# Optimization experiments

Hardware: AMD Instinct MI355X
Metric: run time of the kernel (lower is better)

The kernel has to match this reference:

```python
import jax, jax.numpy as jnp
import numpy as np
from jax import lax

B, C_IN, H, W = 16, 64, 112, 112
OUP = 128
INIT = 64          # ceil(oup/ratio)
NEW = 64           # init*(ratio-1)
E = 4              # num_experts
SE_HID = (INIT + NEW) // 4
EPS = 1e-5


def setup_inputs() -> dict:
    key = jax.random.key(0)
    ks = jax.random.split(key, 12)
    n = jax.random.normal
    d = {}
    d["x"] = n(ks[0], (B, C_IN, H, W), jnp.float32)
    # DynamicConv 1 (1x1, experts)
    d["rw1"] = n(ks[1], (E, C_IN), jnp.float32) * 0.1
    d["rb1"] = jnp.zeros((E,), jnp.float32)
    d["w1"] = n(ks[2], (E, INIT, C_IN, 1, 1), jnp.float32) / np.sqrt(C_IN)
    d["bn1_g"] = jnp.ones((INIT,), jnp.float32)
    d["bn1_b"] = jnp.zeros((INIT,), jnp.float32)
    d["bn1_m"] = n(ks[3], (INIT,), jnp.float32) * 0.1
    d["bn1_v"] = jax.random.uniform(ks[4], (INIT,), jnp.float32, 0.5, 1.5)
    # DynamicConv 2 (3x3 depthwise, experts)
    d["rw2"] = n(ks[5], (E, INIT), jnp.float32) * 0.1
    d["rb2"] = jnp.zeros((E,), jnp.float32)
    d["w2"] = n(ks[6], (E, NEW, 1, 3, 3), jnp.float32) / 3.0
    d["bn2_g"] = jnp.ones((NEW,), jnp.float32)
    d["bn2_b"] = jnp.zeros((NEW,), jnp.float32)
    d["bn2_m"] = n(ks[7], (NEW,), jnp.float32) * 0.1
    d["bn2_v"] = jax.random.uniform(ks[8], (NEW,), jnp.float32, 0.5, 1.5)
    # AdaptiveSE on INIT+NEW channels
    d["se_w1"] = n(ks[9], (SE_HID, INIT + NEW), jnp.float32) * 0.1
    d["se_b1"] = jnp.zeros((SE_HID,), jnp.float32)
    d["se_w2"] = n(ks[10], (INIT + NEW, SE_HID), jnp.float32) * 0.1
    d["se_b2"] = jnp.zeros((INIT + NEW,), jnp.float32)
    return d


def _bn_relu(x, g, b, m, v):
    # eval-mode BatchNorm2d + ReLU, channel dim = 1
    scale = (g / jnp.sqrt(v + EPS))[None, :, None, None]
    shift = (b - m * g / jnp.sqrt(v + EPS))[None, :, None, None]
    return jax.nn.relu(x * scale + shift)


def reference(x, rw1, rb1, w1, bn1_g, bn1_b, bn1_m, bn1_v,
              rw2, rb2, w2, bn2_g, bn2_b, bn2_m, bn2_v,
              se_w1, se_b1, se_w2, se_b2):
    b = x.shape[0]
    # --- first block: dynamic 1x1 conv ---
    pooled = x.mean((2, 3))                                  # [B, C_IN]
    r1 = jax.nn.sigmoid(pooled @ rw1.T + rb1)                # [B, E]
    # per-sample mixed 1x1 kernel: [B, INIT, C_IN]
    k1 = jnp.einsum('be,eoi->boi', r1, w1[:, :, :, 0, 0])
    x1 = jnp.einsum('boi,bihw->bohw', k1, x)                 # [B, INIT, H, W]
    x1 = _bn_relu(x1, bn1_g, bn1_b, bn1_m, bn1_v)
    # --- second block: dynamic 3x3 depthwise conv ---
    pooled2 = x1.mean((2, 3))                                # [B, INIT]
    r2 = jax.nn.sigmoid(pooled2 @ rw2.T + rb2)               # [B, E]
    k2 = jnp.einsum('be,eokl->bokl', r2, w2[:, :, 0])        # [B, NEW, 3, 3]
    # batched grouped conv: groups = B*INIT (CondConv trick)
    x1r = x1.reshape(1, b * INIT, H, W)
    k2r = k2.reshape(b * NEW, 1, 3, 3)
    x2 = lax.conv_general_dilated(
        x1r, k2r, window_strides=(1, 1), padding=((1, 1), (1, 1)),
        dimension_numbers=('NCHW', 'OIHW', 'NCHW'),
        feature_group_count=b * INIT)
    x2 = x2.reshape(b, NEW, H, W)
    x2 = _bn_relu(x2, bn2_g, bn2_b, bn2_m, bn2_v)
    # --- concat + SE gate ---
    out = jnp.concatenate([x1, x2], axis=1)                  # [B, INIT+NEW, H, W]
    s = out.mean((2, 3))                                     # [B, INIT+NEW]
    s = jax.nn.relu(s @ se_w1.T + se_b1)
    s = jax.nn.sigmoid(s @ se_w2.T + se_b2)
    out = out * s[:, :, None, None]
    return out[:, :OUP]
```

## Files before the change

kernel.cpp:

```cpp
#include <hip/hip_runtime.h>
#include <math.h>

#define NB 16
#define CIN 64
#define HH 112
#define WW 112
#define HW 12544
#define INIT_C 64
#define NEW_C 64
#define NE 4
#define SE_HIDN 32
#define OUTC 128
#define EPSV 1e-5f
#define TPX 256
#define NT (HW / TPX)

__global__ __launch_bounds__(256) void k_pool(const float* __restrict__ x,
                                              float* __restrict__ pooled,
                                              float* __restrict__ sum1) {
    int bc = blockIdx.x;
    const float4* p4 = (const float4*)(x + (size_t)bc * HW);
    float s = 0.f;
    for (int g = threadIdx.x; g < HW / 4; g += 256) {
        float4 v = p4[g];
        s += v.x + v.y + v.z + v.w;
    }
    for (int off = 32; off > 0; off >>= 1) s += __shfl_down(s, off, 64);
    __shared__ float ls[4];
    if ((threadIdx.x & 63) == 0) ls[threadIdx.x >> 6] = s;
    __syncthreads();
    if (threadIdx.x == 0) {
        pooled[bc] = (ls[0] + ls[1] + ls[2] + ls[3]) * (1.f / (float)HW);
        sum1[bc] = 0.f;
    }
}

__global__ __launch_bounds__(256) void k_prep(
    const float* __restrict__ pooled, const float* __restrict__ rw1,
    const float* __restrict__ rb1, const float* __restrict__ w1,
    const float* __restrict__ bn1_g, const float* __restrict__ bn1_v,
    float* __restrict__ k1t) {
    int b = blockIdx.x;
    int t = threadIdx.x;
    __shared__ float r1s[NE];
    if (t < NE) {
        float acc = rb1[t];
        const float* pb = pooled + b * CIN;
        const float* rw = rw1 + t * CIN;
        for (int i = 0; i < CIN; i++) acc = fmaf(pb[i], rw[i], acc);
        r1s[t] = 1.f / (1.f + expf(-acc));
    }
    __syncthreads();
    for (int idx = t; idx < CIN * INIT_C; idx += 256) {
        int o = idx & 63, i = idx >> 6;
        float acc = 0.f;
#pragma unroll
        for (int e = 0; e < NE; e++)
            acc = fmaf(r1s[e], w1[(e * INIT_C + o) * CIN + i], acc);
        float sc = bn1_g[o] * rsqrtf(bn1_v[o] + EPSV);
        k1t[b * (CIN * INIT_C) + idx] = acc * sc;
    }
}

__global__ __launch_bounds__(256, 2) void k_conv1(
    const float* __restrict__ x, const float* __restrict__ k1t,
    const float* __restrict__ bn1_g, const float* __restrict__ bn1_b,
    const float* __restrict__ bn1_m, const float* __restrict__ bn1_v,
    float* __restrict__ out, float* __restrict__ sum1) {
    __shared__ alignas(16) float sA[CIN * INIT_C];
    __shared__ alignas(16) float sX[CIN * TPX];
    __shared__ float sShift[INIT_C];
    int b = blockIdx.x / NT;
    int tile = blockIdx.x % NT;
    int p0 = tile * TPX;
    int t = threadIdx.x;

    {
        const float4* src = (const float4*)(k1t + (size_t)b * CIN * INIT_C);
        for (int g = t; g < CIN * INIT_C / 4; g += 256) ((float4*)sA)[g] = src[g];
    }
    if (t < INIT_C) {
        float sc = bn1_g[t] * rsqrtf(bn1_v[t] + EPSV);
        sShift[t] = bn1_b[t] - bn1_m[t] * sc;
    }
    {
        const float* gx = x + (size_t)b * CIN * HW + p0;
        for (int g = t; g < CIN * TPX / 4; g += 256) {
            int i = g >> 6, c4 = g & 63;
            ((float4*)sX)[g] = *(const float4*)(gx + (size_t)i * HW + (c4 << 2));
        }
    }
    __syncthreads();

    int og = t >> 5;
    int pg = t & 31;
    float acc[8][8];
#pragma unroll
    for (int u = 0; u < 8; u++)
#pragma unroll
        for (int v = 0; v < 8; v++) acc[u][v] = 0.f;

    const float4* sA4 = (const float4*)sA;
    const float4* sX4 = (const float4*)sX;
#pragma unroll 2
    for (int i = 0; i < CIN; i++) {
        float4 a0 = sA4[i * (INIT_C / 4) + og * 2];
        float4 a1 = sA4[i * (INIT_C / 4) + og * 2 + 1];
        float4 x0 = sX4[i * (TPX / 4) + pg];
        float4 x1 = sX4[i * (TPX / 4) + 32 + pg];
        float av[8] = {a0.x, a0.y, a0.z, a0.w, a1.x, a1.y, a1.z, a1.w};
        float xv[8] = {x0.x, x0.y, x0.z, x0.w, x1.x, x1.y, x1.z, x1.w};
#pragma unroll
        for (int u = 0; u < 8; u++)
#pragma unroll
            for (int v = 0; v < 8; v++)
                acc[u][v] = fmaf(av[u], xv[v], acc[u][v]);
    }

    float csum[8];
#pragma unroll
    for (int u = 0; u < 8; u++) {
        int o = og * 8 + u;
        float sh = sShift[o];
        alignas(16) float r0[4], r1[4];
#pragma unroll
        for (int v = 0; v < 4; v++) {
            r0[v] = fmaxf(acc[u][v] + sh, 0.f);
            r1[v] = fmaxf(acc[u][4 + v] + sh, 0.f);
        }
        float* dst = out + ((size_t)(b * OUTC + o)) * HW + p0;
        *(float4*)(dst + pg * 4) = *(float4*)r0;
        *(float4*)(dst + 128 + pg * 4) = *(float4*)r1;
        csum[u] = r0[0] + r0[1] + r0[2] + r0[3] + r1[0] + r1[1] + r1[2] + r1[3];
    }
#pragma unroll
    for (int u = 0; u < 8; u++) {
        float v = csum[u];
        v += __shfl_xor(v, 16, 64);
        v += __shfl_xor(v, 8, 64);
        v += __shfl_xor(v, 4, 64);
        v += __shfl_xor(v, 2, 64);
        v += __shfl_xor(v, 1, 64);
        if (pg == 0) atomicAdd(&sum1[b * INIT_C + og * 8 + u], v);
    }
}

__device__ __forceinline__ void ldrow(const float* __restrict__ sP, int pr,
                                      int cg, float4& C, float& L, float& R) {
    const float* row = sP + pr * WW;
    C = *(const float4*)(row + cg * 4);
    int lc = cg * 4 - 1;
    lc = lc < 0 ? 0 : lc;
    float lv = row[lc];
    L = (cg == 0) ? 0.f : lv;
    int rc = cg * 4 + 4;
    rc = rc > (WW - 1) ? (WW - 1) : rc;
    float rv = row[rc];
    R = (cg == 27) ? 0.f : rv;
}

__device__ __forceinline__ float4 dw9(const float4 c0, float l0, float r0,
                                      const float4 c1, float l1, float r1,
                                      const float4 c2, float l2, float r2,
                                      const float* __restrict__ K) {
    float4 o;
    o.x = fmaf(K[0], l0, fmaf(K[1], c0.x, fmaf(K[2], c0.y,
          fmaf(K[3], l1, fmaf(K[4], c1.x, fmaf(K[5], c1.y,
          fmaf(K[6], l2, fmaf(K[7], c2.x, K[8] * c2.y))))))));
    o.y = fmaf(K[0], c0.x, fmaf(K[1], c0.y, fmaf(K[2], c0.z,
          fmaf(K[3], c1.x, fmaf(K[4], c1.y, fmaf(K[5], c1.z,
          fmaf(K[6], c2.x, fmaf(K[7], c2.y, K[8] * c2.z))))))));
    o.z = fmaf(K[0], c0.y, fmaf(K[1], c0.z, fmaf(K[2], c0.w,
          fmaf(K[3], c1.y, fmaf(K[4], c1.z, fmaf(K[5], c1.w,
          fmaf(K[6], c2.y, fmaf(K[7], c2.z, K[8] * c2.w))))))));
    o.w = fmaf(K[0], c0.z, fmaf(K[1], c0.w, fmaf(K[2], r0,
          fmaf(K[3], c1.z, fmaf(K[4], c1.w, fmaf(K[5], r1,
          fmaf(K[6], c2.z, fmaf(K[7], c2.w, K[8] * r2))))))));
    return o;
}

#define PROWS (HH + 2)

__global__ __launch_bounds__(256) void k_dwsum(
    const float* __restrict__ xin, const float* __restrict__ sum1,
    const float* __restrict__ rw2, const float* __restrict__ rb2,
    const float* __restrict__ w2, const float* __restrict__ bn2_g,
    const float* __restrict__ bn2_b, const float* __restrict__ bn2_m,
    const float* __restrict__ bn2_v, float* __restrict__ sum2) {
    __shared__ alignas(16) float sP[PROWS * WW];
    __shared__ float r2s[NE];
    __shared__ float kks[9];
    int c = blockIdx.x & 63;
    int b = blockIdx.x >> 6;
    int t = threadIdx.x;

    if (t < NE) {
        float acc = rb2[t];
        const float* s1 = sum1 + b * INIT_C;
        const float* rw = rw2 + t * INIT_C;
        for (int i = 0; i < INIT_C; i++)
            acc = fmaf(s1[i] * (1.f / (float)HW), rw[i], acc);
        r2s[t] = 1.f / (1.f + expf(-acc));
    }
    if (t < WW / 4) {
        float4 z = {0.f, 0.f, 0.f, 0.f};
        ((float4*)sP)[t] = z;
        ((float4*)(sP + (PROWS - 1) * WW))[t] = z;
    }
    __syncthreads();
    if (t < 9) {
        float acc = 0.f;
#pragma unroll
        for (int e = 0; e < NE; e++)
            acc = fmaf(r2s[e], w2[(e * NEW_C + c) * 9 + t], acc);
        kks[t] = acc * (bn2_g[c] * rsqrtf(bn2_v[c] + EPSV));
    }
    const float4* src4 = (const float4*)(xin + ((size_t)(b * OUTC + c)) * HW);
    float4* dst4 = (float4*)(sP + WW);
    for (int g = t; g < HW / 4; g += 256) dst4[g] = src4[g];
    __syncthreads();

    float sc2 = bn2_g[c] * rsqrtf(bn2_v[c] + EPSV);
    float shift = bn2_b[c] - bn2_m[c] * sc2;
    float myk[9];
#pragma unroll
    for (int j = 0; j < 9; j++) myk[j] = kks[j];

    int cg = t & 31;
    int band = t >> 5;
    float csum = 0.f;
    if (cg < 28) {
        int pr0 = band * 14;
        float4 C[3];
        float L[3], R[3];
        ldrow(sP, pr0, cg, C[0], L[0], R[0]);
        ldrow(sP, pr0 + 1, cg, C[1], L[1], R[1]);
#pragma unroll
        for (int k = 0; k < 14; k++) {
            int s0 = k % 3, s1 = (k + 1) % 3, s2 = (k + 2) % 3;
            ldrow(sP, pr0 + k + 2, cg, C[s2], L[s2], R[s2]);
            float4 o = dw9(C[s0], L[s0], R[s0], C[s1], L[s1], R[s1],
                           C[s2], L[s2], R[s2], myk);
            csum += fmaxf(o.x + shift, 0.f) + fmaxf(o.y + shift, 0.f) +
                    fmaxf(o.z + shift, 0.f) + fmaxf(o.w + shift, 0.f);
        }
    }
    for (int off = 32; off > 0; off >>= 1) csum += __shfl_down(csum, off, 64);
    __shared__ float ls[4];
    if ((t & 63) == 0) ls[t >> 6] = csum;
    __syncthreads();
    if (t == 0) sum2[b * NEW_C + c] = ls[0] + ls[1] + ls[2] + ls[3];
}

__global__ __launch_bounds__(256) void k_final(
    const float* __restrict__ xin, const float* __restrict__ sum1,
    const float* __restrict__ sum2, const float* __restrict__ rw2,
    const float* __restrict__ rb2, const float* __restrict__ w2,
    const float* __restrict__ bn2_g, const float* __restrict__ bn2_b,
    const float* __restrict__ bn2_m, const float* __restrict__ bn2_v,
    const float* __restrict__ se_w1, const float* __restrict__ se_b1,
    const float* __restrict__ se_w2, const float* __restrict__ se_b2,
    float* __restrict__ out) {
    __shared__ alignas(16) float sP[PROWS * WW];
    __shared__ float sin_[OUTC];
    __shared__ float hvec[SE_HIDN];
    __shared__ float r2s[NE];
    __shared__ float kks[9];
    int c = blockIdx.x & 63;
    int b = blockIdx.x >> 6;
    int t = threadIdx.x;

    if (t < 64) sin_[t] = sum1[b * 64 + t] * (1.f / (float)HW);
    else if (t < 128) sin_[t] = sum2[b * 64 + (t - 64)] * (1.f / (float)HW);
    if (t >= 128 && t < 128 + NE) {
        int e = t - 128;
        float acc = rb2[e];
        const float* s1 = sum1 + b * INIT_C;
        const float* rw = rw2 + e * INIT_C;
        for (int i = 0; i < INIT_C; i++)
            acc = fmaf(s1[i] * (1.f / (float)HW), rw[i], acc);
        r2s[e] = 1.f / (1.f + expf(-acc));
    }
    if (t >= 160 && t < 160 + WW / 4) {
        float4 z = {0.f, 0.f, 0.f, 0.f};
        ((float4*)sP)[t - 160] = z;
        ((float4*)(sP + (PROWS - 1) * WW))[t - 160] = z;
    }
    __syncthreads();
    if (t < SE_HIDN) {
        float acc = se_b1[t];
        const float* wrow = se_w1 + t * OUTC;
#pragma unroll 4
        for (int i = 0; i < OUTC; i++) acc = fmaf(sin_[i], wrow[i], acc);
        hvec[t] = fmaxf(acc, 0.f);
    }
    if (t >= 64 && t < 73) {
        int j = t - 64;
        float acc = 0.f;
#pragma unroll
        for (int e = 0; e < NE; e++)
            acc = fmaf(r2s[e], w2[(e * NEW_C + c) * 9 + j], acc);
        kks[j] = acc * (bn2_g[c] * rsqrtf(bn2_v[c] + EPSV));
    }
    const float4* src4 = (const float4*)(xin + ((size_t)(b * OUTC + c)) * HW);
    float4* pdst4 = (float4*)(sP + WW);
    for (int g = t; g < HW / 4; g += 256) pdst4[g] = src4[g];
    __syncthreads();
    float a1 = se_b2[c], a2 = se_b2[64 + c];
    {
        const float* w2a = se_w2 + c * SE_HIDN;
        const float* w2b = se_w2 + (64 + c) * SE_HIDN;
#pragma unroll 8
        for (int j = 0; j < SE_HIDN; j++) {
            float hj = hvec[j];
            a1 = fmaf(hj, w2a[j], a1);
            a2 = fmaf(hj, w2b[j], a2);
        }
    }
    float s1v = 1.f / (1.f + expf(-a1));
    float s2v = 1.f / (1.f + expf(-a2));
    float sc2 = bn2_g[c] * rsqrtf(bn2_v[c] + EPSV);
    float shift = bn2_b[c] - bn2_m[c] * sc2;
    float myk[9];
#pragma unroll
    for (int j = 0; j < 9; j++) myk[j] = kks[j];

    int cg = t & 31;
    int band = t >> 5;
    if (cg < 28) {
        float* d1 = out + ((size_t)(b * OUTC + c)) * HW;
        float* d2 = out + ((size_t)(b * OUTC + 64 + c)) * HW;
        int pr0 = band * 14;
        float4 C[3];
        float L[3], R[3];
        ldrow(sP, pr0, cg, C[0], L[0], R[0]);
        ldrow(sP, pr0 + 1, cg, C[1], L[1], R[1]);
#pragma unroll
        for (int k = 0; k < 14; k++) {
            int s0 = k % 3, s1 = (k + 1) % 3, s2 = (k + 2) % 3;
            ldrow(sP, pr0 + k + 2, cg, C[s2], L[s2], R[s2]);
            float4 o = dw9(C[s0], L[s0], R[s0], C[s1], L[s1], R[s1],
                           C[s2], L[s2], R[s2], myk);
            float4 x1v = C[s1];
            float4 o1, o2;
            o1.x = x1v.x * s1v; o1.y = x1v.y * s1v;
            o1.z = x1v.z * s1v; o1.w = x1v.w * s1v;
            o2.x = fmaxf(o.x + shift, 0.f) * s2v;
            o2.y = fmaxf(o.y + shift, 0.f) * s2v;
            o2.z = fmaxf(o.z + shift, 0.f) * s2v;
            o2.w = fmaxf(o.w + shift, 0.f) * s2v;
            int row = band * 14 + k;
            *(float4*)(d1 + (size_t)row * WW + cg * 4) = o1;
            *(float4*)(d2 + (size_t)row * WW + cg * 4) = o2;
        }
    }
}

extern "C" void kernel_launch(void* const* d_in, const int* in_sizes, int n_in,
                              void* d_out, int out_size, void* d_ws,
                              size_t ws_size, hipStream_t stream) {
    (void)in_sizes; (void)n_in; (void)out_size; (void)ws_size;
    const float* x = (const float*)d_in[0];
    const float* rw1 = (const float*)d_in[1];
    const float* rb1 = (const float*)d_in[2];
    const float* w1 = (const float*)d_in[3];
    const float* bn1_g = (const float*)d_in[4];
    const float* bn1_b = (const float*)d_in[5];
    const float* bn1_m = (const float*)d_in[6];
    const float* bn1_v = (const float*)d_in[7];
    const float* rw2 = (const float*)d_in[8];
    const float* rb2 = (const float*)d_in[9];
    const float* w2 = (const float*)d_in[10];
    const float* bn2_g = (const float*)d_in[11];
    const float* bn2_b = (const float*)d_in[12];
    const float* bn2_m = (const float*)d_in[13];
    const float* bn2_v = (const float*)d_in[14];
    const float* se_w1 = (const float*)d_in[15];
    const float* se_b1 = (const float*)d_in[16];
    const float* se_w2 = (const float*)d_in[17];
    const float* se_b2 = (const float*)d_in[18];
    float* out = (float*)d_out;
    float* ws = (float*)d_ws;
    float* pooled = ws;
    float* sum1 = ws + 1024;
    float* sum2 = ws + 2048;
    float* k1t = ws + 3072;

    k_pool<<<NB * CIN, 256, 0, stream>>>(x, pooled, sum1);
    k_prep<<<NB, 256, 0, stream>>>(pooled, rw1, rb1, w1, bn1_g, bn1_v, k1t);
    k_conv1<<<NB * NT, 256, 0, stream>>>(x, k1t, bn1_g, bn1_b, bn1_m, bn1_v,
                                         out, sum1);
    k_dwsum<<<NB * NEW_C, 256, 0, stream>>>(out, sum1, rw2, rb2, w2, bn2_g,
                                            bn2_b, bn2_m, bn2_v, sum2);
    k_final<<<NB * NEW_C, 256, 0, stream>>>(out, sum1, sum2, rw2, rb2, w2,
                                            bn2_g, bn2_b, bn2_m, bn2_v, se_w1,
                                            se_b1, se_w2, se_b2, out);
}
```

Baseline: 307.6 us.

## Drop LDS staging in 1x1 conv; read weights via wave-uniform scalar loads

```diff
diff --git a/kernel.cpp b/kernel.cpp
--- a/kernel.cpp
+++ b/kernel.cpp
@@ -38,11 +38,13 @@
 __global__ __launch_bounds__(256) void k_prep(
     const float* __restrict__ pooled, const float* __restrict__ rw1,
     const float* __restrict__ rb1, const float* __restrict__ w1,
-    const float* __restrict__ bn1_g, const float* __restrict__ bn1_v,
-    float* __restrict__ k1t) {
+    const float* __restrict__ bn1_g, const float* __restrict__ bn1_b,
+    const float* __restrict__ bn1_m, const float* __restrict__ bn1_v,
+    float* __restrict__ k1t, float* __restrict__ shift1) {
     int b = blockIdx.x;
     int t = threadIdx.x;
     __shared__ float r1s[NE];
+    __shared__ float sT[64][65];
     if (t < NE) {
         float acc = rb1[t];
         const float* pb = pooled + b * CIN;
@@ -50,98 +52,78 @@
         for (int i = 0; i < CIN; i++) acc = fmaf(pb[i], rw[i], acc);
         r1s[t] = 1.f / (1.f + expf(-acc));
     }
+    if (t >= 64 && t < 128) {
+        int o = t - 64;
+        float sc = bn1_g[o] * rsqrtf(bn1_v[o] + EPSV);
+        shift1[o] = bn1_b[o] - bn1_m[o] * sc;
+    }
     __syncthreads();
     for (int idx = t; idx < CIN * INIT_C; idx += 256) {
-        int o = idx & 63, i = idx >> 6;
+        int o = idx >> 6, i = idx & 63;
         float acc = 0.f;
 #pragma unroll
         for (int e = 0; e < NE; e++)
             acc = fmaf(r1s[e], w1[(e * INIT_C + o) * CIN + i], acc);
         float sc = bn1_g[o] * rsqrtf(bn1_v[o] + EPSV);
-        k1t[b * (CIN * INIT_C) + idx] = acc * sc;
-    }
-}
-
-__global__ __launch_bounds__(256, 2) void k_conv1(
+        sT[o][i] = acc * sc;
+    }
+    __syncthreads();
+    for (int idx = t; idx < CIN * INIT_C; idx += 256) {
+        int i = idx >> 6, o = idx & 63;
+        k1t[(b << 12) + idx] = sT[o][i];
+    }
+}
+
+__global__ __launch_bounds__(256, 4) void k_conv1(
     const float* __restrict__ x, const float* __restrict__ k1t,
-    const float* __restrict__ bn1_g, const float* __restrict__ bn1_b,
-    const float* __restrict__ bn1_m, const float* __restrict__ bn1_v,
-    float* __restrict__ out, float* __restrict__ sum1) {
-    __shared__ alignas(16) float sA[CIN * INIT_C];
-    __shared__ alignas(16) float sX[CIN * TPX];
-    __shared__ float sShift[INIT_C];
+    const float* __restrict__ shift1, float* __restrict__ out,
+    float* __restrict__ sum1) {
     int b = blockIdx.x / NT;
-    int tile = blockIdx.x % NT;
+    int tile = blockIdx.x - b * NT;
     int p0 = tile * TPX;
     int t = threadIdx.x;
-
-    {
-        const float4* src = (const float4*)(k1t + (size_t)b * CIN * INIT_C);
-        for (int g = t; g < CIN * INIT_C / 4; g += 256) ((float4*)sA)[g] = src[g];
-    }
-    if (t < INIT_C) {
-        float sc = bn1_g[t] * rsqrtf(bn1_v[t] + EPSV);
-        sShift[t] = bn1_b[t] - bn1_m[t] * sc;
-    }
-    {
-        const float* gx = x + (size_t)b * CIN * HW + p0;
-        for (int g = t; g < CIN * TPX / 4; g += 256) {
-            int i = g >> 6, c4 = g & 63;
-            ((float4*)sX)[g] = *(const float4*)(gx + (size_t)i * HW + (c4 << 2));
-        }
-    }
-    __syncthreads();
-
-    int og = t >> 5;
-    int pg = t & 31;
-    float acc[8][8];
-#pragma unroll
-    for (int u = 0; u < 8; u++)
-#pragma unroll
-        for (int v = 0; v < 8; v++) acc[u][v] = 0.f;
-
-    const float4* sA4 = (const float4*)sA;
-    const float4* sX4 = (const float4*)sX;
+    int lane = t & 63;
+    int og16 = __builtin_amdgcn_readfirstlane(t >> 6) << 4;
+    const float* Aw = k1t + (b << 12) + og16;
+    float shv[16];
+#pragma unroll
+    for (int j = 0; j < 16; j++) shv[j] = shift1[og16 + j];
+
+    const float* xp = x + (size_t)(b * CIN) * HW + p0 + (lane << 2);
+    float4 acc[16];
+#pragma unroll
+    for (int j = 0; j < 16; j++) acc[j] = make_float4(0.f, 0.f, 0.f, 0.f);
+
 #pragma unroll 2
     for (int i = 0; i < CIN; i++) {
-        float4 a0 = sA4[i * (INIT_C / 4) + og * 2];
-        float4 a1 = sA4[i * (INIT_C / 4) + og * 2 + 1];
-        float4 x0 = sX4[i * (TPX / 4) + pg];
-        float4 x1 = sX4[i * (TPX / 4) + 32 + pg];
-        float av[8] = {a0.x, a0.y, a0.z, a0.w, a1.x, a1.y, a1.z, a1.w};
-        float xv[8] = {x0.x, x0.y, x0.z, x0.w, x1.x, x1.y, x1.z, x1.w};
-#pragma unroll
-        for (int u = 0; u < 8; u++)
-#pragma unroll
-            for (int v = 0; v < 8; v++)
-                acc[u][v] = fmaf(av[u], xv[v], acc[u][v]);
-    }
-
-    float csum[8];
-#pragma unroll
-    for (int u = 0; u < 8; u++) {
-        int o = og * 8 + u;
-        float sh = sShift[o];
-        alignas(16) float r0[4], r1[4];
-#pragma unroll
-        for (int v = 0; v < 4; v++) {
-            r0[v] = fmaxf(acc[u][v] + sh, 0.f);
-            r1[v] = fmaxf(acc[u][4 + v] + sh, 0.f);
+        float4 xv = *(const float4*)(xp + (size_t)i * HW);
+#pragma unroll
+        for (int j = 0; j < 16; j++) {
+            float a = Aw[i * 64 + j];
+            acc[j].x = fmaf(a, xv.x, acc[j].x);
+            acc[j].y = fmaf(a, xv.y, acc[j].y);
+            acc[j].z = fmaf(a, xv.z, acc[j].z);
+            acc[j].w = fmaf(a, xv.w, acc[j].w);
         }
-        float* dst = out + ((size_t)(b * OUTC + o)) * HW + p0;
-        *(float4*)(dst + pg * 4) = *(float4*)r0;
-        *(float4*)(dst + 128 + pg * 4) = *(float4*)r1;
-        csum[u] = r0[0] + r0[1] + r0[2] + r0[3] + r1[0] + r1[1] + r1[2] + r1[3];
-    }
-#pragma unroll
-    for (int u = 0; u < 8; u++) {
-        float v = csum[u];
-        v += __shfl_xor(v, 16, 64);
-        v += __shfl_xor(v, 8, 64);
-        v += __shfl_xor(v, 4, 64);
-        v += __shfl_xor(v, 2, 64);
-        v += __shfl_xor(v, 1, 64);
-        if (pg == 0) atomicAdd(&sum1[b * INIT_C + og * 8 + u], v);
+    }
+
+    float* outbase = out + ((size_t)(b * OUTC + og16)) * HW + p0 + (lane << 2);
+#pragma unroll
+    for (int j = 0; j < 16; j++) {
+        float4 r;
+        r.x = fmaxf(acc[j].x + shv[j], 0.f);
+        r.y = fmaxf(acc[j].y + shv[j], 0.f);
+        r.z = fmaxf(acc[j].z + shv[j], 0.f);
+        r.w = fmaxf(acc[j].w + shv[j], 0.f);
+        *(float4*)(outbase + (size_t)j * HW) = r;
+        float cs = r.x + r.y + r.z + r.w;
+        cs += __shfl_xor(cs, 1, 64);
+        cs += __shfl_xor(cs, 2, 64);
+        cs += __shfl_xor(cs, 4, 64);
+        cs += __shfl_xor(cs, 8, 64);
+        cs += __shfl_xor(cs, 16, 64);
+        cs += __shfl_xor(cs, 32, 64);
+        if (lane == 0) atomicAdd(&sum1[b * INIT_C + og16 + j], cs);
     }
 }
 
@@ -384,12 +366,13 @@
     float* pooled = ws;
     float* sum1 = ws + 1024;
     float* sum2 = ws + 2048;
-    float* k1t = ws + 3072;
+    float* shift1 = ws + 3072;
+    float* k1t = ws + 4096;
 
     k_pool<<<NB * CIN, 256, 0, stream>>>(x, pooled, sum1);
-    k_prep<<<NB, 256, 0, stream>>>(pooled, rw1, rb1, w1, bn1_g, bn1_v, k1t);
-    k_conv1<<<NB * NT, 256, 0, stream>>>(x, k1t, bn1_g, bn1_b, bn1_m, bn1_v,
-                                         out, sum1);
+    k_prep<<<NB, 256, 0, stream>>>(pooled, rw1, rb1, w1, bn1_g, bn1_b, bn1_m,
+                                   bn1_v, k1t, shift1);
+    k_conv1<<<NB * NT, 256, 0, stream>>>(x, k1t, shift1, out, sum1);
     k_dwsum<<<NB * NEW_C, 256, 0, stream>>>(out, sum1, rw2, rb2, w2, bn2_g,
                                             bn2_b, bn2_m, bn2_v, sum2);
     k_final<<<NB * NEW_C, 256, 0, stream>>>(out, sum1, sum2, rw2, rb2, w2,
```

Measured after the change: 285.3 us. -7.2%, faster.
